# Kernel tuning notes

Measured on AMD Instinct MI355X. Metric: run time of the kernel, lower is better.

The kernel has to match this reference:

```python
import jax, jax.numpy as jnp
import numpy as np

TOP_K = 12
OBS_RADIUS = 1.0
DIST_MIN_THRES = 0.8
EPS = 1e-4


def setup_inputs() -> dict:
    key = jax.random.key(0)
    ks = jax.random.split(key, 9)
    N, in_dim = 4096, 4
    c = in_dim + 2  # pairwise diff + eye flag + (dist - thres)
    states = jax.random.normal(ks[0], (N, in_dim), dtype=jnp.float32) * 2.0
    def w(k, o, i):
        return jax.random.normal(k, (o, i), dtype=jnp.float32) * (1.0 / np.sqrt(i))
    return {
        "states": states,
        "W1": w(ks[1], 64, c),  "b1": jnp.zeros((64,), jnp.float32),
        "W2": w(ks[2], 128, 64), "b2": jnp.zeros((128,), jnp.float32),
        "W3": w(ks[3], 64, 128), "b3": jnp.zeros((64,), jnp.float32),
        "W4": w(ks[4], 1, 64),   "b4": jnp.zeros((1,), jnp.float32),
    }


def _conv1x1(h, W, b):
    # h: [N, C_in, L]; 1x1 Conv1d == channel matmul
    return jnp.einsum('oi,nil->nol', W, h) + b[None, :, None]


def reference(states, W1, b1, W2, b2, W3, b3, W4, b4):
    N = states.shape[0]
    # pairwise differences: [N, N, in_dim]
    x = states[:, None, :] - states[None, :, :]
    d_norm = jnp.sqrt(jnp.sum(jnp.square(x[:, :, :2]) + EPS, axis=2))  # [N, N]
    eye = jnp.eye(N, dtype=x.dtype)
    x = jnp.concatenate(
        [x, eye[:, :, None], (d_norm - DIST_MIN_THRES)[:, :, None]], axis=2
    )  # [N, N, c]
    # remove_distant_agents: keep TOP_K nearest neighbors per agent
    dn = jnp.sqrt(jnp.sum(jnp.square(x[:, :, :2]) + EPS, axis=2))  # [N, N]
    _, idx = jax.lax.top_k(-dn, TOP_K)                              # [N, k]
    x = jnp.take_along_axis(x, idx[:, :, None], axis=1)            # [N, k, c]
    dist = jnp.sqrt(jnp.sum(jnp.square(x[:, :, :2]) + EPS, axis=2, keepdims=True))  # [N,k,1]
    k, c = x.shape[1], x.shape[2]
    mask = (dist <= OBS_RADIUS).astype(x.dtype).reshape(-1, 1, k)  # [N,1,k] (reshape, as in source)
    h = x.reshape(-1, c, k)  # faithful: source uses reshape, NOT transpose
    h = jax.nn.relu(_conv1x1(h, W1, b1))
    h = jax.nn.relu(_conv1x1(h, W2, b2))
    h = jax.nn.relu(_conv1x1(h, W3, b3))
    h = _conv1x1(h, W4, b4)  # [N, 1, k]
    h = h * mask
    return h, mask
```

## Files before the change

### kernel.cpp

```cpp
#include <hip/hip_runtime.h>
#include <stdint.h>

#define NAG 4096
#define TOPK 12
#define EPSF 1e-4f
#define NT 256
#define WPB 4
#define MTOT (NAG * TOPK)

typedef unsigned long long u64;
typedef short short8v __attribute__((ext_vector_type(8)));
typedef float f32x4 __attribute__((ext_vector_type(4)));

__device__ __forceinline__ u64 umin64(u64 a, u64 b) { return a < b ? a : b; }

__device__ __forceinline__ unsigned short f2bf(float f) {
    union { float f; unsigned u; } v; v.f = f;
    unsigned r = v.u + 0x7FFFu + ((v.u >> 16) & 1u);
    return (unsigned short)(r >> 16);
}

template <int CTRL>
__device__ __forceinline__ void dpp_min_step(unsigned &hi, unsigned &lo) {
    unsigned ohi = (unsigned)__builtin_amdgcn_update_dpp((int)hi, (int)hi, CTRL, 0xf, 0xf, false);
    unsigned olo = (unsigned)__builtin_amdgcn_update_dpp((int)lo, (int)lo, CTRL, 0xf, 0xf, false);
    bool t = (ohi < hi) || (ohi == hi && olo < lo);
    hi = t ? ohi : hi;
    lo = t ? olo : lo;
}

__global__ __launch_bounds__(NT, 4)
void cbf_select(const float* __restrict__ states,
                float* __restrict__ xbuf,
                float* __restrict__ out)
{
    const int t = threadIdx.x;
    const int lane = t & 63;
    const int wv = t >> 6;
    const int i = blockIdx.x * WPB + wv;

    __shared__ u64 s_surv[WPB][64];
    __shared__ int s_sel[WPB][TOPK];
    __shared__ float s_x[WPB][72];

    const float2* st2 = reinterpret_cast<const float2*>(states);
    const float si0 = states[i * 4 + 0];
    const float si1 = states[i * 4 + 1];

    unsigned dnb[64];
    unsigned minb = 0xFFFFFFFFu;
    int minj = 0;
#pragma unroll
    for (int u = 0; u < 64; ++u) {
        int j = u * 64 + lane;
        float2 sj = st2[j * 2];
        float dx0 = __fsub_rn(si0, sj.x);
        float dx1 = __fsub_rn(si1, sj.y);
        float d2 = __fadd_rn(__fadd_rn(__fmul_rn(dx0, dx0), EPSF),
                             __fadd_rn(__fmul_rn(dx1, dx1), EPSF));
        unsigned b = __float_as_uint(__fsqrt_rn(d2));
        dnb[u] = b;
        if (b < minb) { minb = b; minj = j; }
    }

    unsigned Tb;
    {
        unsigned khi = minb, klo = (unsigned)minj;
        unsigned Tcur = 0;
        for (int r = 0; r < TOPK; ++r) {
            unsigned hi = khi, lo = klo;
            dpp_min_step<0xB1>(hi, lo);
            dpp_min_step<0x4E>(hi, lo);
            dpp_min_step<0x124>(hi, lo);
            dpp_min_step<0x128>(hi, lo);
            dpp_min_step<0x142>(hi, lo);
            dpp_min_step<0x143>(hi, lo);
            unsigned hw = (unsigned)__builtin_amdgcn_readlane((int)hi, 63);
            unsigned lw = (unsigned)__builtin_amdgcn_readlane((int)lo, 63);
            Tcur = hw;
            if (khi == hw && klo == lw) khi = 0xFFFFFFFFu;
        }
        Tb = Tcur;
    }

    int cnt = 0;
#pragma unroll
    for (int u = 0; u < 64; ++u) {
        bool p = (dnb[u] <= Tb);
        u64 mk = __ballot(p);
        if (p) {
            int pos = cnt + __popcll(mk & ((1ull << lane) - 1ull));
            if (pos < 64)
                s_surv[wv][pos] = ((u64)dnb[u] << 32) | (unsigned)(u * 64 + lane);
        }
        cnt += __popcll(mk);
    }
    if (cnt > 64) cnt = 64;
    __asm volatile("s_waitcnt lgkmcnt(0)" ::: "memory");
    __builtin_amdgcn_wave_barrier();

    if (lane < cnt) {
        u64 kA = s_surv[wv][lane];
        int rA = 0;
        for (int q = 0; q < cnt; ++q)
            rA += (s_surv[wv][q] < kA) ? 1 : 0;
        if (rA < TOPK) s_sel[wv][rA] = (int)(unsigned)(kA & 0xffffffffull);
    }
    __asm volatile("s_waitcnt lgkmcnt(0)" ::: "memory");
    __builtin_amdgcn_wave_barrier();

    if (lane < TOPK) {
        int j = s_sel[wv][lane];
        const float4 sj = reinterpret_cast<const float4*>(states)[j];
        const float4 si = reinterpret_cast<const float4*>(states)[i];
        float dx0 = __fsub_rn(si.x, sj.x);
        float dx1 = __fsub_rn(si.y, sj.y);
        float dx2 = __fsub_rn(si.z, sj.z);
        float dx3 = __fsub_rn(si.w, sj.w);
        float d2 = __fadd_rn(__fadd_rn(__fmul_rn(dx0, dx0), EPSF),
                             __fadd_rn(__fmul_rn(dx1, dx1), EPSF));
        float dn = __fsqrt_rn(d2);
        s_x[wv][lane * 6 + 0] = dx0;
        s_x[wv][lane * 6 + 1] = dx1;
        s_x[wv][lane * 6 + 2] = dx2;
        s_x[wv][lane * 6 + 3] = dx3;
        s_x[wv][lane * 6 + 4] = (j == i) ? 1.0f : 0.0f;
        s_x[wv][lane * 6 + 5] = __fsub_rn(dn, 0.8f);
        out[MTOT + i * TOPK + lane] = (dn <= 1.0f) ? 1.0f : 0.0f;
    }
    __asm volatile("s_waitcnt lgkmcnt(0)" ::: "memory");
    __builtin_amdgcn_wave_barrier();

    if (lane < TOPK) {
        int m = i * TOPK + lane;
        float4 v0 = {s_x[wv][0 * 12 + lane], s_x[wv][1 * 12 + lane],
                     s_x[wv][2 * 12 + lane], s_x[wv][3 * 12 + lane]};
        float4 v1 = {s_x[wv][4 * 12 + lane], s_x[wv][5 * 12 + lane], 0.0f, 0.0f};
        reinterpret_cast<float4*>(xbuf + m * 8)[0] = v0;
        reinterpret_cast<float4*>(xbuf + m * 8)[1] = v1;
    }
}

__global__ __launch_bounds__(256)
void cbf_mlp(const float* __restrict__ xbuf,
             const float* __restrict__ W1, const float* __restrict__ b1,
             const float* __restrict__ W2, const float* __restrict__ b2,
             const float* __restrict__ W3, const float* __restrict__ b3,
             const float* __restrict__ W4, const float* __restrict__ b4,
             float* __restrict__ out)
{
    const int t = threadIdx.x;
    const int lane = t & 63;
    const int wv = t >> 6;
    const int r16 = lane & 15;
    const int hi = lane >> 4;
    const int m0 = blockIdx.x * 64 + wv * 16;

    __shared__ __align__(16) unsigned char s_h1[4 * 2048];
    __shared__ __align__(16) unsigned char s_h2[4 * 4096];
    unsigned char* lp1 = s_h1 + wv * 2048;
    unsigned char* lp2 = s_h2 + wv * 4096;

    const int mrow = m0 + r16;
    const float4 xa = reinterpret_cast<const float4*>(xbuf + mrow * 8)[0];
    const float4 xb = reinterpret_cast<const float4*>(xbuf + mrow * 8)[1];
    const float xc[6] = {xa.x, xa.y, xa.z, xa.w, xb.x, xb.y};

    unsigned short h1b[16];
#pragma unroll
    for (int ol = 0; ol < 16; ++ol) {
        int o = hi * 16 + ol;
        const float2* wr = reinterpret_cast<const float2*>(W1 + o * 6);
        float2 w0 = wr[0], w1 = wr[1], w2 = wr[2];
        float acc = b1[o];
        acc = fmaf(w0.x, xc[0], acc);
        acc = fmaf(w0.y, xc[1], acc);
        acc = fmaf(w1.x, xc[2], acc);
        acc = fmaf(w1.y, xc[3], acc);
        acc = fmaf(w2.x, xc[4], acc);
        acc = fmaf(w2.y, xc[5], acc);
        h1b[ol] = f2bf(fmaxf(acc, 0.0f));
    }
    {
        short8v p0, p1;
#pragma unroll
        for (int e = 0; e < 8; ++e) { p0[e] = (short)h1b[e]; p1[e] = (short)h1b[8 + e]; }
        int rowb = r16 * 128;
        *(short8v*)(lp1 + rowb + (((2 * hi + 0) ^ (r16 & 7)) * 16)) = p0;
        *(short8v*)(lp1 + rowb + (((2 * hi + 1) ^ (r16 & 7)) * 16)) = p1;
    }
    __syncthreads();

    short8v a0 = *(short8v*)(lp1 + r16 * 128 + (((0 + hi) ^ (r16 & 7)) * 16));
    short8v a1 = *(short8v*)(lp1 + r16 * 128 + (((4 + hi) ^ (r16 & 7)) * 16));
    const int c = r16;
#pragma unroll
    for (int nt = 0; nt < 8; ++nt) {
        const float* wrow = W2 + (nt * 16 + c) * 64;
        float4 g0 = *(const float4*)(wrow + 8 * hi);
        float4 g1 = *(const float4*)(wrow + 8 * hi + 4);
        float4 g2 = *(const float4*)(wrow + 32 + 8 * hi);
        float4 g3 = *(const float4*)(wrow + 36 + 8 * hi);
        short8v bf0, bf1;
        bf0[0] = (short)f2bf(g0.x); bf0[1] = (short)f2bf(g0.y);
        bf0[2] = (short)f2bf(g0.z); bf0[3] = (short)f2bf(g0.w);
        bf0[4] = (short)f2bf(g1.x); bf0[5] = (short)f2bf(g1.y);
        bf0[6] = (short)f2bf(g1.z); bf0[7] = (short)f2bf(g1.w);
        bf1[0] = (short)f2bf(g2.x); bf1[1] = (short)f2bf(g2.y);
        bf1[2] = (short)f2bf(g2.z); bf1[3] = (short)f2bf(g2.w);
        bf1[4] = (short)f2bf(g3.x); bf1[5] = (short)f2bf(g3.y);
        bf1[6] = (short)f2bf(g3.z); bf1[7] = (short)f2bf(g3.w);
        float bb = b2[nt * 16 + c];
        f32x4 acc = {bb, bb, bb, bb};
        acc = __builtin_amdgcn_mfma_f32_16x16x32_bf16(a0, bf0, acc, 0, 0, 0);
        acc = __builtin_amdgcn_mfma_f32_16x16x32_bf16(a1, bf1, acc, 0, 0, 0);
#pragma unroll
        for (int e = 0; e < 4; ++e) {
            unsigned short hv = f2bf(fmaxf(acc[e], 0.0f));
            int mr = 4 * hi + e;
            int slot = (2 * nt + (c >> 3)) ^ (mr & 15);
            *(unsigned short*)(lp2 + mr * 256 + slot * 16 + ((2 * c) & 15)) = hv;
        }
    }
    __syncthreads();

    short8v a3[4];
#pragma unroll
    for (int ks = 0; ks < 4; ++ks)
        a3[ks] = *(short8v*)(lp2 + r16 * 256 + (((4 * ks + hi) ^ r16) * 16));
    float h3r[4][4];
#pragma unroll
    for (int nt = 0; nt < 4; ++nt) {
        const float* wrow = W3 + (nt * 16 + c) * 128;
        float bb = b3[nt * 16 + c];
        f32x4 ac = {bb, bb, bb, bb};
#pragma unroll
        for (int ks = 0; ks < 4; ++ks) {
            float4 q0 = *(const float4*)(wrow + ks * 32 + 8 * hi);
            float4 q1 = *(const float4*)(wrow + ks * 32 + 8 * hi + 4);
            short8v bf;
            bf[0] = (short)f2bf(q0.x); bf[1] = (short)f2bf(q0.y);
            bf[2] = (short)f2bf(q0.z); bf[3] = (short)f2bf(q0.w);
            bf[4] = (short)f2bf(q1.x); bf[5] = (short)f2bf(q1.y);
            bf[6] = (short)f2bf(q1.z); bf[7] = (short)f2bf(q1.w);
            ac = __builtin_amdgcn_mfma_f32_16x16x32_bf16(a3[ks], bf, ac, 0, 0, 0);
        }
#pragma unroll
        for (int e = 0; e < 4; ++e) h3r[nt][e] = fmaxf(ac[e], 0.0f);
    }

    float w4c[4];
#pragma unroll
    for (int nt = 0; nt < 4; ++nt) w4c[nt] = W4[nt * 16 + c];
    float part[4];
#pragma unroll
    for (int e = 0; e < 4; ++e) {
        float p = h3r[0][e] * w4c[0];
        p = fmaf(h3r[1][e], w4c[1], p);
        p = fmaf(h3r[2][e], w4c[2], p);
        p = fmaf(h3r[3][e], w4c[3], p);
        part[e] = p;
    }
#pragma unroll
    for (int off = 1; off <= 8; off <<= 1) {
#pragma unroll
        for (int e = 0; e < 4; ++e)
            part[e] += __shfl_xor(part[e], off, 64);
    }
    if (c == 0) {
        float bb4 = b4[0];
#pragma unroll
        for (int e = 0; e < 4; ++e) {
            int m = m0 + 4 * hi + e;
            float mk = out[MTOT + m];
            out[m] = (part[e] + bb4) * mk;
        }
    }
}

extern "C" void kernel_launch(void* const* d_in, const int* in_sizes, int n_in,
                              void* d_out, int out_size, void* d_ws, size_t ws_size,
                              hipStream_t stream) {
    const float* states = (const float*)d_in[0];
    const float* W1 = (const float*)d_in[1];
    const float* b1 = (const float*)d_in[2];
    const float* W2 = (const float*)d_in[3];
    const float* b2 = (const float*)d_in[4];
    const float* W3 = (const float*)d_in[5];
    const float* b3 = (const float*)d_in[6];
    const float* W4 = (const float*)d_in[7];
    const float* b4 = (const float*)d_in[8];
    float* out = (float*)d_out;
    float* xbuf = (float*)d_ws;

    cbf_select<<<dim3(NAG / WPB), dim3(NT), 0, stream>>>(states, xbuf, out);
    cbf_mlp<<<dim3(MTOT / 64), dim3(256), 0, stream>>>(xbuf, W1, b1, W2, b2,
                                                       W3, b3, W4, b4, out);
}
```

Measured before the change: 122.7 us.

## Fuse neighbor selection and MLP into one kernel with pre-converted bf16 weights

Merges the top-k selection kernel and the MLP kernel into a single kernel, so each wave runs the MLP on its own agent's 12 neighbors directly from shared memory. This removes the xbuf round trip and the reread of the mask. Agent xy positions are staged in LDS once per block. Distances are recomputed in a second pass instead of being held in 64 registers, trading extra ALU work for lower register pressure. W2 and W3 are converted to bf16 once by a small prep kernel instead of in every wave, and the block grows to 8 waves. The costs are MFMA rows padded from 12 to 16, so 4 of 16 rows are wasted, plus an extra kernel launch.

```diff
diff --git a/kernel.cpp b/kernel.cpp
--- a/kernel.cpp
+++ b/kernel.cpp
@@ -4,15 +4,14 @@
 #define NAG 4096
 #define TOPK 12
 #define EPSF 1e-4f
-#define NT 256
-#define WPB 4
+#define NT 512
+#define WPB 8
+#define NBLK (NAG / WPB)
 #define MTOT (NAG * TOPK)
 
 typedef unsigned long long u64;
 typedef short short8v __attribute__((ext_vector_type(8)));
 typedef float f32x4 __attribute__((ext_vector_type(4)));
-
-__device__ __forceinline__ u64 umin64(u64 a, u64 b) { return a < b ? a : b; }
 
 __device__ __forceinline__ unsigned short f2bf(float f) {
     union { float f; unsigned u; } v; v.f = f;
@@ -29,38 +28,56 @@
     lo = t ? olo : lo;
 }
 
+__global__ __launch_bounds__(256)
+void cbf_prep(const float* __restrict__ W2, const float* __restrict__ W3,
+              unsigned short* __restrict__ Wb) {
+    int idx = blockIdx.x * 256 + threadIdx.x;
+    float v = (idx < 8192) ? W2[idx] : W3[idx - 8192];
+    Wb[idx] = f2bf(v);
+}
+
 __global__ __launch_bounds__(NT, 4)
-void cbf_select(const float* __restrict__ states,
-                float* __restrict__ xbuf,
-                float* __restrict__ out)
+void cbf_fused(const float* __restrict__ states,
+               const float* __restrict__ W1, const float* __restrict__ b1,
+               const unsigned short* __restrict__ Wb,
+               const float* __restrict__ b2, const float* __restrict__ b3,
+               const float* __restrict__ W4, const float* __restrict__ b4,
+               float* __restrict__ out)
 {
     const int t = threadIdx.x;
     const int lane = t & 63;
     const int wv = t >> 6;
     const int i = blockIdx.x * WPB + wv;
 
+    __shared__ float2 s_xy[NAG];
     __shared__ u64 s_surv[WPB][64];
     __shared__ int s_sel[WPB][TOPK];
     __shared__ float s_x[WPB][72];
-
-    const float2* st2 = reinterpret_cast<const float2*>(states);
-    const float si0 = states[i * 4 + 0];
-    const float si1 = states[i * 4 + 1];
-
-    unsigned dnb[64];
+    __shared__ float s_mask[WPB][TOPK];
+    __shared__ __align__(16) unsigned char s_h2[WPB][4096];
+
+#pragma unroll
+    for (int u = 0; u < 8; ++u) {
+        int r = u * NT + t;
+        float4 sr = reinterpret_cast<const float4*>(states)[r];
+        s_xy[r] = make_float2(sr.x, sr.y);
+    }
+    __syncthreads();
+
+    const float2 sif = s_xy[i];
+    const float si0 = sif.x, si1 = sif.y;
+
     unsigned minb = 0xFFFFFFFFu;
     int minj = 0;
-#pragma unroll
+#pragma unroll 8
     for (int u = 0; u < 64; ++u) {
-        int j = u * 64 + lane;
-        float2 sj = st2[j * 2];
+        float2 sj = s_xy[u * 64 + lane];
         float dx0 = __fsub_rn(si0, sj.x);
         float dx1 = __fsub_rn(si1, sj.y);
         float d2 = __fadd_rn(__fadd_rn(__fmul_rn(dx0, dx0), EPSF),
                              __fadd_rn(__fmul_rn(dx1, dx1), EPSF));
         unsigned b = __float_as_uint(__fsqrt_rn(d2));
-        dnb[u] = b;
-        if (b < minb) { minb = b; minj = j; }
+        if (b < minb) { minb = b; minj = u * 64 + lane; }
     }
 
     unsigned Tb;
@@ -84,14 +101,20 @@
     }
 
     int cnt = 0;
-#pragma unroll
+#pragma unroll 8
     for (int u = 0; u < 64; ++u) {
-        bool p = (dnb[u] <= Tb);
+        float2 sj = s_xy[u * 64 + lane];
+        float dx0 = __fsub_rn(si0, sj.x);
+        float dx1 = __fsub_rn(si1, sj.y);
+        float d2 = __fadd_rn(__fadd_rn(__fmul_rn(dx0, dx0), EPSF),
+                             __fadd_rn(__fmul_rn(dx1, dx1), EPSF));
+        unsigned b = __float_as_uint(__fsqrt_rn(d2));
+        bool p = (b <= Tb);
         u64 mk = __ballot(p);
         if (p) {
             int pos = cnt + __popcll(mk & ((1ull << lane) - 1ull));
             if (pos < 64)
-                s_surv[wv][pos] = ((u64)dnb[u] << 32) | (unsigned)(u * 64 + lane);
+                s_surv[wv][pos] = ((u64)b << 32) | (unsigned)(u * 64 + lane);
         }
         cnt += __popcll(mk);
     }
@@ -126,91 +149,61 @@
         s_x[wv][lane * 6 + 3] = dx3;
         s_x[wv][lane * 6 + 4] = (j == i) ? 1.0f : 0.0f;
         s_x[wv][lane * 6 + 5] = __fsub_rn(dn, 0.8f);
-        out[MTOT + i * TOPK + lane] = (dn <= 1.0f) ? 1.0f : 0.0f;
-    }
-    __asm volatile("s_waitcnt lgkmcnt(0)" ::: "memory");
-    __builtin_amdgcn_wave_barrier();
-
-    if (lane < TOPK) {
-        int m = i * TOPK + lane;
-        float4 v0 = {s_x[wv][0 * 12 + lane], s_x[wv][1 * 12 + lane],
-                     s_x[wv][2 * 12 + lane], s_x[wv][3 * 12 + lane]};
-        float4 v1 = {s_x[wv][4 * 12 + lane], s_x[wv][5 * 12 + lane], 0.0f, 0.0f};
-        reinterpret_cast<float4*>(xbuf + m * 8)[0] = v0;
-        reinterpret_cast<float4*>(xbuf + m * 8)[1] = v1;
-    }
-}
-
-__global__ __launch_bounds__(256)
-void cbf_mlp(const float* __restrict__ xbuf,
-             const float* __restrict__ W1, const float* __restrict__ b1,
-             const float* __restrict__ W2, const float* __restrict__ b2,
-             const float* __restrict__ W3, const float* __restrict__ b3,
-             const float* __restrict__ W4, const float* __restrict__ b4,
-             float* __restrict__ out)
-{
-    const int t = threadIdx.x;
-    const int lane = t & 63;
-    const int wv = t >> 6;
+        float mk = (dn <= 1.0f) ? 1.0f : 0.0f;
+        s_mask[wv][lane] = mk;
+        out[MTOT + i * TOPK + lane] = mk;
+    }
+    __asm volatile("s_waitcnt lgkmcnt(0)" ::: "memory");
+    __builtin_amdgcn_wave_barrier();
+
     const int r16 = lane & 15;
     const int hi = lane >> 4;
-    const int m0 = blockIdx.x * 64 + wv * 16;
-
-    __shared__ __align__(16) unsigned char s_h1[4 * 2048];
-    __shared__ __align__(16) unsigned char s_h2[4 * 4096];
-    unsigned char* lp1 = s_h1 + wv * 2048;
-    unsigned char* lp2 = s_h2 + wv * 4096;
-
-    const int mrow = m0 + r16;
-    const float4 xa = reinterpret_cast<const float4*>(xbuf + mrow * 8)[0];
-    const float4 xb = reinterpret_cast<const float4*>(xbuf + mrow * 8)[1];
-    const float xc[6] = {xa.x, xa.y, xa.z, xa.w, xb.x, xb.y};
-
-    unsigned short h1b[16];
-#pragma unroll
-    for (int ol = 0; ol < 16; ++ol) {
-        int o = hi * 16 + ol;
-        const float2* wr = reinterpret_cast<const float2*>(W1 + o * 6);
-        float2 w0 = wr[0], w1 = wr[1], w2 = wr[2];
-        float acc = b1[o];
-        acc = fmaf(w0.x, xc[0], acc);
-        acc = fmaf(w0.y, xc[1], acc);
-        acc = fmaf(w1.x, xc[2], acc);
-        acc = fmaf(w1.y, xc[3], acc);
-        acc = fmaf(w2.x, xc[4], acc);
-        acc = fmaf(w2.y, xc[5], acc);
-        h1b[ol] = f2bf(fmaxf(acc, 0.0f));
-    }
-    {
-        short8v p0, p1;
-#pragma unroll
-        for (int e = 0; e < 8; ++e) { p0[e] = (short)h1b[e]; p1[e] = (short)h1b[8 + e]; }
-        int rowb = r16 * 128;
-        *(short8v*)(lp1 + rowb + (((2 * hi + 0) ^ (r16 & 7)) * 16)) = p0;
-        *(short8v*)(lp1 + rowb + (((2 * hi + 1) ^ (r16 & 7)) * 16)) = p1;
-    }
-    __syncthreads();
-
-    short8v a0 = *(short8v*)(lp1 + r16 * 128 + (((0 + hi) ^ (r16 & 7)) * 16));
-    short8v a1 = *(short8v*)(lp1 + r16 * 128 + (((4 + hi) ^ (r16 & 7)) * 16));
+
+    float xc[6];
+#pragma unroll
+    for (int ch = 0; ch < 6; ++ch)
+        xc[ch] = (r16 < TOPK) ? s_x[wv][ch * TOPK + r16] : 0.0f;
+
+    short8v a0, a1;
+#pragma unroll
+    for (int e = 0; e < 8; ++e) {
+        {
+            int o = 8 * hi + e;
+            const float2* wr = reinterpret_cast<const float2*>(W1 + o * 6);
+            float2 w0 = wr[0], w1 = wr[1], w2 = wr[2];
+            float acc = b1[o];
+            acc = fmaf(w0.x, xc[0], acc);
+            acc = fmaf(w0.y, xc[1], acc);
+            acc = fmaf(w1.x, xc[2], acc);
+            acc = fmaf(w1.y, xc[3], acc);
+            acc = fmaf(w2.x, xc[4], acc);
+            acc = fmaf(w2.y, xc[5], acc);
+            a0[e] = (r16 < TOPK) ? (short)f2bf(fmaxf(acc, 0.0f)) : (short)0;
+        }
+        {
+            int o = 32 + 8 * hi + e;
+            const float2* wr = reinterpret_cast<const float2*>(W1 + o * 6);
+            float2 w0 = wr[0], w1 = wr[1], w2 = wr[2];
+            float acc = b1[o];
+            acc = fmaf(w0.x, xc[0], acc);
+            acc = fmaf(w0.y, xc[1], acc);
+            acc = fmaf(w1.x, xc[2], acc);
+            acc = fmaf(w1.y, xc[3], acc);
+            acc = fmaf(w2.x, xc[4], acc);
+            acc = fmaf(w2.y, xc[5], acc);
+            a1[e] = (r16 < TOPK) ? (short)f2bf(fmaxf(acc, 0.0f)) : (short)0;
+        }
+    }
+
+    unsigned char* lp2 = s_h2[wv];
     const int c = r16;
+
 #pragma unroll
     for (int nt = 0; nt < 8; ++nt) {
-        const float* wrow = W2 + (nt * 16 + c) * 64;
-        float4 g0 = *(const float4*)(wrow + 8 * hi);
-        float4 g1 = *(const float4*)(wrow + 8 * hi + 4);
-        float4 g2 = *(const float4*)(wrow + 32 + 8 * hi);
-        float4 g3 = *(const float4*)(wrow + 36 + 8 * hi);
-        short8v bf0, bf1;
-        bf0[0] = (short)f2bf(g0.x); bf0[1] = (short)f2bf(g0.y);
-        bf0[2] = (short)f2bf(g0.z); bf0[3] = (short)f2bf(g0.w);
-        bf0[4] = (short)f2bf(g1.x); bf0[5] = (short)f2bf(g1.y);
-        bf0[6] = (short)f2bf(g1.z); bf0[7] = (short)f2bf(g1.w);
-        bf1[0] = (short)f2bf(g2.x); bf1[1] = (short)f2bf(g2.y);
-        bf1[2] = (short)f2bf(g2.z); bf1[3] = (short)f2bf(g2.w);
-        bf1[4] = (short)f2bf(g3.x); bf1[5] = (short)f2bf(g3.y);
-        bf1[6] = (short)f2bf(g3.z); bf1[7] = (short)f2bf(g3.w);
-        float bb = b2[nt * 16 + c];
+        int o = nt * 16 + c;
+        short8v bf0 = *(const short8v*)(Wb + o * 64 + 8 * hi);
+        short8v bf1 = *(const short8v*)(Wb + o * 64 + 32 + 8 * hi);
+        float bb = b2[o];
         f32x4 acc = {bb, bb, bb, bb};
         acc = __builtin_amdgcn_mfma_f32_16x16x32_bf16(a0, bf0, acc, 0, 0, 0);
         acc = __builtin_amdgcn_mfma_f32_16x16x32_bf16(a1, bf1, acc, 0, 0, 0);
@@ -222,7 +215,8 @@
             *(unsigned short*)(lp2 + mr * 256 + slot * 16 + ((2 * c) & 15)) = hv;
         }
     }
-    __syncthreads();
+    __asm volatile("s_waitcnt lgkmcnt(0)" ::: "memory");
+    __builtin_amdgcn_wave_barrier();
 
     short8v a3[4];
 #pragma unroll
@@ -231,18 +225,12 @@
     float h3r[4][4];
 #pragma unroll
     for (int nt = 0; nt < 4; ++nt) {
-        const float* wrow = W3 + (nt * 16 + c) * 128;
-        float bb = b3[nt * 16 + c];
+        int o = nt * 16 + c;
+        float bb = b3[o];
         f32x4 ac = {bb, bb, bb, bb};
 #pragma unroll
         for (int ks = 0; ks < 4; ++ks) {
-            float4 q0 = *(const float4*)(wrow + ks * 32 + 8 * hi);
-            float4 q1 = *(const float4*)(wrow + ks * 32 + 8 * hi + 4);
-            short8v bf;
-            bf[0] = (short)f2bf(q0.x); bf[1] = (short)f2bf(q0.y);
-            bf[2] = (short)f2bf(q0.z); bf[3] = (short)f2bf(q0.w);
-            bf[4] = (short)f2bf(q1.x); bf[5] = (short)f2bf(q1.y);
-            bf[6] = (short)f2bf(q1.z); bf[7] = (short)f2bf(q1.w);
+            short8v bf = *(const short8v*)(Wb + 8192 + o * 128 + ks * 32 + 8 * hi);
             ac = __builtin_amdgcn_mfma_f32_16x16x32_bf16(a3[ks], bf, ac, 0, 0, 0);
         }
 #pragma unroll
@@ -271,9 +259,9 @@
         float bb4 = b4[0];
 #pragma unroll
         for (int e = 0; e < 4; ++e) {
-            int m = m0 + 4 * hi + e;
-            float mk = out[MTOT + m];
-            out[m] = (part[e] + bb4) * mk;
+            int mr = 4 * hi + e;
+            if (mr < TOPK)
+                out[i * TOPK + mr] = (part[e] + bb4) * s_mask[wv][mr];
         }
     }
 }
@@ -291,9 +279,9 @@
     const float* W4 = (const float*)d_in[7];
     const float* b4 = (const float*)d_in[8];
     float* out = (float*)d_out;
-    float* xbuf = (float*)d_ws;
-
-    cbf_select<<<dim3(NAG / WPB), dim3(NT), 0, stream>>>(states, xbuf, out);
-    cbf_mlp<<<dim3(MTOT / 64), dim3(256), 0, stream>>>(xbuf, W1, b1, W2, b2,
-                                                       W3, b3, W4, b4, out);
-}
+    unsigned short* Wb = (unsigned short*)d_ws;
+
+    cbf_prep<<<dim3(64), dim3(256), 0, stream>>>(W2, W3, Wb);
+    cbf_fused<<<dim3(NBLK), dim3(NT), 0, stream>>>(states, W1, b1, Wb,
+                                                   b2, b3, W4, b4, out);
+}
```

New measurement: 103.1 us. -16.0%, faster.
